# Optimization experiments

Hardware: AMD Instinct MI355X
Metric: run time of the kernel (lower is better)

Reference implementation:

```python
import jax, jax.numpy as jnp
import numpy as np

C_M, C_Z, NUM_BINS = 256, 128, 15
MIN_BIN, MAX_BIN, INF = 3.25, 20.75, 1e8
EPS = 1e-5


def _layer_norm(x, gamma, beta):
    mu = jnp.mean(x, axis=-1, keepdims=True)
    var = jnp.mean(jnp.square(x - mu), axis=-1, keepdims=True)
    return (x - mu) * jax.lax.rsqrt(var + EPS) * gamma + beta


def setup_inputs() -> dict:
    key = jax.random.key(0)
    ks = jax.random.split(key, 8)
    B, NC, NR = 1, 128, 512
    m = jax.random.normal(ks[0], (B, NC, NR, C_M), dtype=jnp.float32)
    z = jax.random.normal(ks[1], (B, NR, NR, C_Z), dtype=jnp.float32)
    m0_prev = jax.random.normal(ks[2], (B, NR, C_M), dtype=jnp.float32)
    z_prev = jax.random.normal(ks[3], (B, NR, NR, C_Z), dtype=jnp.float32)
    # scale coords so pairwise distances span the [3.25, 20.75] Angstrom bins
    x_prev = jax.random.normal(ks[4], (B, NR, 3), dtype=jnp.float32) * 8.0
    w = jax.random.normal(ks[5], (C_Z, NUM_BINS), dtype=jnp.float32) * 0.1
    b = jax.random.normal(ks[6], (C_Z,), dtype=jnp.float32) * 0.1
    gamma_m = jnp.ones((C_M,), jnp.float32)
    beta_m = jnp.zeros((C_M,), jnp.float32)
    gamma_z = jnp.ones((C_Z,), jnp.float32)
    beta_z = jnp.zeros((C_Z,), jnp.float32)
    return {"m": m, "z": z, "m0_prev": m0_prev, "z_prev": z_prev, "x_prev": x_prev,
            "w": w, "b": b, "gamma_m": gamma_m, "beta_m": beta_m,
            "gamma_z": gamma_z, "beta_z": beta_z}


def reference(m, z, m0_prev, z_prev, x_prev, w, b, gamma_m, beta_m, gamma_z, beta_z):
    dtype = x_prev.dtype
    bins = jnp.linspace(MIN_BIN, MAX_BIN, NUM_BINS, dtype=dtype)
    lower = jnp.square(bins)                                  # [num_bins]
    upper = jnp.concatenate([lower[1:], jnp.array([INF], dtype=dtype)])
    # pairwise squared distances -> one-hot bin -> linear embed
    diff = x_prev[:, :, None, :] - x_prev[:, None, :, :]      # [B,N,N,3]
    d2 = jnp.sum(jnp.square(diff), axis=-1, keepdims=True)    # [B,N,N,1]
    onehot = ((d2 > lower) & (d2 < upper)).astype(dtype)      # [B,N,N,num_bins]
    d = jnp.einsum('bijk,ck->bijc', onehot, w) + b            # [B,N,N,c_z]
    z_update = _layer_norm(z_prev, gamma_z, beta_z)
    m0_update = _layer_norm(m0_prev, gamma_m, beta_m)
    m_out = m.at[:, 0].add(m0_update)
    z_out = z + z_update + d
    return m_out, z_out
```

## Files before the change

### kernel.cpp

```cpp
#include <hip/hip_runtime.h>

#define NR 512
#define NC 128
#define CM 256
#define CZ 128
#define NBINS 15

typedef float f32x4 __attribute__((ext_vector_type(4)));

#define NTLOAD(p)     __builtin_nontemporal_load(p)
#define NTSTORE(p, v) __builtin_nontemporal_store((v), (p))

#define ZBLOCKS (NR * NR / 8)
#define MTOTAL4 (NC * NR * CM / 4)
#define MBLOCKS (MTOTAL4 / 512)
#define SLICE4  (NR * CM / 4)
#define MSLICEBLOCKS (SLICE4 / 512)

__global__ void __launch_bounds__(256) fused_kernel(
        const f32x4* __restrict__ m,
        const float* __restrict__ z,
        const f32x4* __restrict__ m0prev,
        const float* __restrict__ zprev,
        const float* __restrict__ xprev,
        const float* __restrict__ w,
        const f32x4* __restrict__ bvec4,
        const f32x4* __restrict__ gm4,
        const f32x4* __restrict__ bm4,
        const f32x4* __restrict__ gz4,
        const f32x4* __restrict__ bz4,
        f32x4* __restrict__ mout,
        float* __restrict__ zout) {
    const int bid = blockIdx.x;
    const int t   = threadIdx.x;

    if (bid < ZBLOCKS) {
        const int half = t >> 5;
        const int lane = t & 31;
        const long long row  = (long long)bid * 8 + half;
        const int i = (int)(row >> 9);
        const int j = (int)(row & (NR - 1));
        const long long base = row * CZ + lane * 4;

        const f32x4 zp = NTLOAD((const f32x4*)(zprev + base));
        const f32x4 zv = NTLOAD((const f32x4*)(z + base));

        float s  = zp.x + zp.y + zp.z + zp.w;
        float ss = zp.x*zp.x + zp.y*zp.y + zp.z*zp.z + zp.w*zp.w;
        #pragma unroll
        for (int msk = 1; msk < 32; msk <<= 1) {
            s  += __shfl_xor(s,  msk);
            ss += __shfl_xor(ss, msk);
        }
        const float mu  = s * (1.0f / CZ);
        const float var = ss * (1.0f / CZ) - mu * mu;
        const float inv = rsqrtf(var + 1e-5f);

        const float dx = __fsub_rn(xprev[i * 3 + 0], xprev[j * 3 + 0]);
        const float dy = __fsub_rn(xprev[i * 3 + 1], xprev[j * 3 + 1]);
        const float dz = __fsub_rn(xprev[i * 3 + 2], xprev[j * 3 + 2]);
        const float d2 = __fadd_rn(__fadd_rn(__fmul_rn(dx, dx), __fmul_rn(dy, dy)),
                                   __fmul_rn(dz, dz));

        int bin = -1;
        #pragma unroll
        for (int k = 0; k < NBINS; k++) {
            const float bk = 3.25f + 1.25f * (float)k;
            const float lo = bk * bk;
            const float up = (k == NBINS - 1) ? 1e8f
                            : (3.25f + 1.25f * (float)(k + 1)) * (3.25f + 1.25f * (float)(k + 1));
            if (d2 > lo && d2 < up) bin = k;
        }

        const int c0 = lane * 4;
        const f32x4 g  = gz4[lane];
        const f32x4 be = bz4[lane];
        const f32x4 bb = bvec4[lane];

        float w0 = 0.f, w1 = 0.f, w2 = 0.f, w3 = 0.f;
        if (bin >= 0) {
            w0 = w[(c0 + 0) * NBINS + bin];
            w1 = w[(c0 + 1) * NBINS + bin];
            w2 = w[(c0 + 2) * NBINS + bin];
            w3 = w[(c0 + 3) * NBINS + bin];
        }

        f32x4 o;
        o.x = (zv.x + ((zp.x - mu) * inv * g.x + be.x)) + (w0 + bb.x);
        o.y = (zv.y + ((zp.y - mu) * inv * g.y + be.y)) + (w1 + bb.y);
        o.z = (zv.z + ((zp.z - mu) * inv * g.z + be.z)) + (w2 + bb.z);
        o.w = (zv.w + ((zp.w - mu) * inv * g.w + be.w)) + (w3 + bb.w);
        NTSTORE((f32x4*)(zout + base), o);
    } else {
        const int mb   = bid - ZBLOCKS;
        const int idx0 = mb * 512 + t;
        const int idx1 = idx0 + 256;

        f32x4 v0 = NTLOAD(m + idx0);
        f32x4 v1 = NTLOAD(m + idx1);

        if (mb < MSLICEBLOCKS) {
            const int lane = t & 63;
            const f32x4 g  = gm4[lane];
            const f32x4 be = bm4[lane];
            #pragma unroll
            for (int e = 0; e < 2; e++) {
                const int idx = e ? idx1 : idx0;
                const f32x4 mp = m0prev[idx];
                float s  = mp.x + mp.y + mp.z + mp.w;
                float ss = mp.x*mp.x + mp.y*mp.y + mp.z*mp.z + mp.w*mp.w;
                #pragma unroll
                for (int msk = 1; msk < 64; msk <<= 1) {
                    s  += __shfl_xor(s,  msk);
                    ss += __shfl_xor(ss, msk);
                }
                const float mu  = s * (1.0f / CM);
                const float var = ss * (1.0f / CM) - mu * mu;
                const float inv = rsqrtf(var + 1e-5f);
                f32x4& v = e ? v1 : v0;
                v.x += (mp.x - mu) * inv * g.x + be.x;
                v.y += (mp.y - mu) * inv * g.y + be.y;
                v.z += (mp.z - mu) * inv * g.z + be.z;
                v.w += (mp.w - mu) * inv * g.w + be.w;
            }
        }
        NTSTORE(mout + idx0, v0);
        NTSTORE(mout + idx1, v1);
    }
}

extern "C" void kernel_launch(void* const* d_in, const int* in_sizes, int n_in,
                              void* d_out, int out_size, void* d_ws, size_t ws_size,
                              hipStream_t stream) {
    const float* m      = (const float*)d_in[0];
    const float* z      = (const float*)d_in[1];
    const float* m0prev = (const float*)d_in[2];
    const float* zprev  = (const float*)d_in[3];
    const float* xprev  = (const float*)d_in[4];
    const float* w      = (const float*)d_in[5];
    const float* b      = (const float*)d_in[6];
    const float* gm     = (const float*)d_in[7];
    const float* bm     = (const float*)d_in[8];
    const float* gz     = (const float*)d_in[9];
    const float* bz     = (const float*)d_in[10];

    float* mout = (float*)d_out;
    float* zout = (float*)d_out + (size_t)NC * NR * CM;

    fused_kernel<<<ZBLOCKS + MBLOCKS, 256, 0, stream>>>(
        (const f32x4*)m, z, (const f32x4*)m0prev, zprev, xprev, w,
        (const f32x4*)b, (const f32x4*)gm, (const f32x4*)bm,
        (const f32x4*)gz, (const f32x4*)bz,
        (f32x4*)mout, zout);
}
```

Baseline: 103.9 us.

## Process two z rows and four m vectors per thread; drop nontemporal loads

Each thread in the z path now handles two pair rows (j and j+8) instead of one, and each m-path thread copies four vectors instead of two. This halves the block count and gives each thread more loads in flight. The separate upper-bound check in binning is replaced by a cumulative count of lower bounds crossed, and nontemporal loads become plain loads. The binning rewrite assumes d2 never equals a bin edge exactly, and the plain loads may change cache behaviour for this streaming workload.

```diff
diff --git a/kernel.cpp b/kernel.cpp
--- a/kernel.cpp
+++ b/kernel.cpp
@@ -8,14 +8,12 @@
 
 typedef float f32x4 __attribute__((ext_vector_type(4)));
 
-#define NTLOAD(p)     __builtin_nontemporal_load(p)
 #define NTSTORE(p, v) __builtin_nontemporal_store((v), (p))
 
-#define ZBLOCKS (NR * NR / 8)
+#define ZBLOCKS (NR * NR / 16)
 #define MTOTAL4 (NC * NR * CM / 4)
-#define MBLOCKS (MTOTAL4 / 512)
-#define SLICE4  (NR * CM / 4)
-#define MSLICEBLOCKS (SLICE4 / 512)
+#define MBLOCKS (MTOTAL4 / 1024)
+#define MSLICEBLOCKS (NR * CM / 4 / 1024)
 
 __global__ void __launch_bounds__(256) fused_kernel(
         const f32x4* __restrict__ m,
@@ -37,39 +35,54 @@
     if (bid < ZBLOCKS) {
         const int half = t >> 5;
         const int lane = t & 31;
-        const long long row  = (long long)bid * 8 + half;
-        const int i = (int)(row >> 9);
-        const int j = (int)(row & (NR - 1));
-        const long long base = row * CZ + lane * 4;
+        const int row0 = bid * 16 + half;
+        const int row1 = row0 + 8;
+        const long long base0 = (long long)row0 * CZ + lane * 4;
+        const long long base1 = (long long)row1 * CZ + lane * 4;
 
-        const f32x4 zp = NTLOAD((const f32x4*)(zprev + base));
-        const f32x4 zv = NTLOAD((const f32x4*)(z + base));
+        const f32x4 zp0 = *(const f32x4*)(zprev + base0);
+        const f32x4 zp1 = *(const f32x4*)(zprev + base1);
+        const f32x4 zv0 = *(const f32x4*)(z + base0);
+        const f32x4 zv1 = *(const f32x4*)(z + base1);
 
-        float s  = zp.x + zp.y + zp.z + zp.w;
-        float ss = zp.x*zp.x + zp.y*zp.y + zp.z*zp.z + zp.w*zp.w;
+        float s0  = zp0.x + zp0.y + zp0.z + zp0.w;
+        float ss0 = zp0.x*zp0.x + zp0.y*zp0.y + zp0.z*zp0.z + zp0.w*zp0.w;
+        float s1  = zp1.x + zp1.y + zp1.z + zp1.w;
+        float ss1 = zp1.x*zp1.x + zp1.y*zp1.y + zp1.z*zp1.z + zp1.w*zp1.w;
         #pragma unroll
         for (int msk = 1; msk < 32; msk <<= 1) {
-            s  += __shfl_xor(s,  msk);
-            ss += __shfl_xor(ss, msk);
+            s0  += __shfl_xor(s0,  msk);
+            ss0 += __shfl_xor(ss0, msk);
+            s1  += __shfl_xor(s1,  msk);
+            ss1 += __shfl_xor(ss1, msk);
         }
-        const float mu  = s * (1.0f / CZ);
-        const float var = ss * (1.0f / CZ) - mu * mu;
-        const float inv = rsqrtf(var + 1e-5f);
+        const float mu0  = s0 * (1.0f / CZ);
+        const float inv0 = rsqrtf(ss0 * (1.0f / CZ) - mu0 * mu0 + 1e-5f);
+        const float mu1  = s1 * (1.0f / CZ);
+        const float inv1 = rsqrtf(ss1 * (1.0f / CZ) - mu1 * mu1 + 1e-5f);
 
-        const float dx = __fsub_rn(xprev[i * 3 + 0], xprev[j * 3 + 0]);
-        const float dy = __fsub_rn(xprev[i * 3 + 1], xprev[j * 3 + 1]);
-        const float dz = __fsub_rn(xprev[i * 3 + 2], xprev[j * 3 + 2]);
-        const float d2 = __fadd_rn(__fadd_rn(__fmul_rn(dx, dx), __fmul_rn(dy, dy)),
-                                   __fmul_rn(dz, dz));
+        const int i  = row0 >> 9;
+        const int j0 = row0 & (NR - 1);
+        const int j1 = j0 + 8;
+        const float xi0 = xprev[i * 3 + 0], xi1 = xprev[i * 3 + 1], xi2 = xprev[i * 3 + 2];
+        const float dx0 = __fsub_rn(xi0, xprev[j0 * 3 + 0]);
+        const float dy0 = __fsub_rn(xi1, xprev[j0 * 3 + 1]);
+        const float dz0 = __fsub_rn(xi2, xprev[j0 * 3 + 2]);
+        const float d2a = __fadd_rn(__fadd_rn(__fmul_rn(dx0, dx0), __fmul_rn(dy0, dy0)),
+                                    __fmul_rn(dz0, dz0));
+        const float dx1 = __fsub_rn(xi0, xprev[j1 * 3 + 0]);
+        const float dy1 = __fsub_rn(xi1, xprev[j1 * 3 + 1]);
+        const float dz1 = __fsub_rn(xi2, xprev[j1 * 3 + 2]);
+        const float d2b = __fadd_rn(__fadd_rn(__fmul_rn(dx1, dx1), __fmul_rn(dy1, dy1)),
+                                    __fmul_rn(dz1, dz1));
 
-        int bin = -1;
+        int bina = -1, binb = -1;
         #pragma unroll
         for (int k = 0; k < NBINS; k++) {
             const float bk = 3.25f + 1.25f * (float)k;
             const float lo = bk * bk;
-            const float up = (k == NBINS - 1) ? 1e8f
-                            : (3.25f + 1.25f * (float)(k + 1)) * (3.25f + 1.25f * (float)(k + 1));
-            if (d2 > lo && d2 < up) bin = k;
+            bina += (d2a > lo) ? 1 : 0;
+            binb += (d2b > lo) ? 1 : 0;
         }
 
         const int c0 = lane * 4;
@@ -77,35 +90,48 @@
         const f32x4 be = bz4[lane];
         const f32x4 bb = bvec4[lane];
 
-        float w0 = 0.f, w1 = 0.f, w2 = 0.f, w3 = 0.f;
-        if (bin >= 0) {
-            w0 = w[(c0 + 0) * NBINS + bin];
-            w1 = w[(c0 + 1) * NBINS + bin];
-            w2 = w[(c0 + 2) * NBINS + bin];
-            w3 = w[(c0 + 3) * NBINS + bin];
+        float wa0 = 0.f, wa1 = 0.f, wa2 = 0.f, wa3 = 0.f;
+        if (bina >= 0) {
+            wa0 = w[(c0 + 0) * NBINS + bina];
+            wa1 = w[(c0 + 1) * NBINS + bina];
+            wa2 = w[(c0 + 2) * NBINS + bina];
+            wa3 = w[(c0 + 3) * NBINS + bina];
+        }
+        float wb0 = 0.f, wb1 = 0.f, wb2 = 0.f, wb3 = 0.f;
+        if (binb >= 0) {
+            wb0 = w[(c0 + 0) * NBINS + binb];
+            wb1 = w[(c0 + 1) * NBINS + binb];
+            wb2 = w[(c0 + 2) * NBINS + binb];
+            wb3 = w[(c0 + 3) * NBINS + binb];
         }
 
-        f32x4 o;
-        o.x = (zv.x + ((zp.x - mu) * inv * g.x + be.x)) + (w0 + bb.x);
-        o.y = (zv.y + ((zp.y - mu) * inv * g.y + be.y)) + (w1 + bb.y);
-        o.z = (zv.z + ((zp.z - mu) * inv * g.z + be.z)) + (w2 + bb.z);
-        o.w = (zv.w + ((zp.w - mu) * inv * g.w + be.w)) + (w3 + bb.w);
-        NTSTORE((f32x4*)(zout + base), o);
+        f32x4 o0, o1;
+        o0.x = (zv0.x + ((zp0.x - mu0) * inv0 * g.x + be.x)) + (wa0 + bb.x);
+        o0.y = (zv0.y + ((zp0.y - mu0) * inv0 * g.y + be.y)) + (wa1 + bb.y);
+        o0.z = (zv0.z + ((zp0.z - mu0) * inv0 * g.z + be.z)) + (wa2 + bb.z);
+        o0.w = (zv0.w + ((zp0.w - mu0) * inv0 * g.w + be.w)) + (wa3 + bb.w);
+        o1.x = (zv1.x + ((zp1.x - mu1) * inv1 * g.x + be.x)) + (wb0 + bb.x);
+        o1.y = (zv1.y + ((zp1.y - mu1) * inv1 * g.y + be.y)) + (wb1 + bb.y);
+        o1.z = (zv1.z + ((zp1.z - mu1) * inv1 * g.z + be.z)) + (wb2 + bb.z);
+        o1.w = (zv1.w + ((zp1.w - mu1) * inv1 * g.w + be.w)) + (wb3 + bb.w);
+        NTSTORE((f32x4*)(zout + base0), o0);
+        NTSTORE((f32x4*)(zout + base1), o1);
     } else {
         const int mb   = bid - ZBLOCKS;
-        const int idx0 = mb * 512 + t;
-        const int idx1 = idx0 + 256;
+        const int idx0 = mb * 1024 + t;
 
-        f32x4 v0 = NTLOAD(m + idx0);
-        f32x4 v1 = NTLOAD(m + idx1);
+        f32x4 v0 = m[idx0];
+        f32x4 v1 = m[idx0 + 256];
+        f32x4 v2 = m[idx0 + 512];
+        f32x4 v3 = m[idx0 + 768];
 
         if (mb < MSLICEBLOCKS) {
             const int lane = t & 63;
             const f32x4 g  = gm4[lane];
             const f32x4 be = bm4[lane];
             #pragma unroll
-            for (int e = 0; e < 2; e++) {
-                const int idx = e ? idx1 : idx0;
+            for (int e = 0; e < 4; e++) {
+                const int idx = idx0 + e * 256;
                 const f32x4 mp = m0prev[idx];
                 float s  = mp.x + mp.y + mp.z + mp.w;
                 float ss = mp.x*mp.x + mp.y*mp.y + mp.z*mp.z + mp.w*mp.w;
@@ -115,17 +141,18 @@
                     ss += __shfl_xor(ss, msk);
                 }
                 const float mu  = s * (1.0f / CM);
-                const float var = ss * (1.0f / CM) - mu * mu;
-                const float inv = rsqrtf(var + 1e-5f);
-                f32x4& v = e ? v1 : v0;
+                const float inv = rsqrtf(ss * (1.0f / CM) - mu * mu + 1e-5f);
+                f32x4& v = (e == 0) ? v0 : (e == 1) ? v1 : (e == 2) ? v2 : v3;
                 v.x += (mp.x - mu) * inv * g.x + be.x;
                 v.y += (mp.y - mu) * inv * g.y + be.y;
                 v.z += (mp.z - mu) * inv * g.z + be.z;
                 v.w += (mp.w - mu) * inv * g.w + be.w;
             }
         }
-        NTSTORE(mout + idx0, v0);
-        NTSTORE(mout + idx1, v1);
+        NTSTORE(mout + idx0,       v0);
+        NTSTORE(mout + idx0 + 256, v1);
+        NTSTORE(mout + idx0 + 512, v2);
+        NTSTORE(mout + idx0 + 768, v3);
     }
 }
 
```

Result: faster. 100.1 us (-3.7%).
